# Optimization experiments

Measured on AMD Instinct MI355X. Metric: run time of the kernel, lower is better.

The kernel has to match this reference:

```python
import jax, jax.numpy as jnp
import numpy as np

NUM_VARS = 64
EDGE_TYPES = 4
HID = 128
IN = 32
BATCH = 64
SKIP_FIRST = True


def setup_inputs() -> dict:
    key = jax.random.key(0)
    ks = jax.random.split(key, 16)
    adj = np.ones((NUM_VARS, NUM_VARS)) - np.eye(NUM_VARS)
    send, recv = np.where(adj)  # [N*(N-1)] each
    E = send.shape[0]
    s = 0.05
    return {
        'inputs': jax.random.normal(ks[0], (BATCH, NUM_VARS, IN), jnp.float32),
        'edges': jax.random.uniform(ks[1], (BATCH, E, EDGE_TYPES), dtype=jnp.float32),
        'msg_fc1_w': jax.random.normal(ks[2], (EDGE_TYPES, HID, 2 * IN), jnp.float32) * s,
        'msg_fc1_b': jax.random.normal(ks[3], (EDGE_TYPES, HID), jnp.float32) * s,
        'msg_fc2_w': jax.random.normal(ks[4], (EDGE_TYPES, HID, HID), jnp.float32) * s,
        'msg_fc2_b': jax.random.normal(ks[5], (EDGE_TYPES, HID), jnp.float32) * s,
        'out_fc1_w': jax.random.normal(ks[6], (HID, IN + HID), jnp.float32) * s,
        'out_fc1_b': jax.random.normal(ks[7], (HID,), jnp.float32) * s,
        'out_fc2_w': jax.random.normal(ks[8], (HID, HID), jnp.float32) * s,
        'out_fc2_b': jax.random.normal(ks[9], (HID,), jnp.float32) * s,
        'mu_w': jax.random.normal(ks[10], (IN, HID), jnp.float32) * s,
        'mu_b': jax.random.normal(ks[11], (IN,), jnp.float32) * s,
        'logstd_w': jax.random.normal(ks[12], (IN, HID), jnp.float32) * s,
        'logstd_b': jax.random.normal(ks[13], (IN,), jnp.float32) * s,
        'send_edges': jnp.asarray(send, jnp.int32),
        'recv_edges': jnp.asarray(recv, jnp.int32),
    }


def reference(inputs, edges, msg_fc1_w, msg_fc1_b, msg_fc2_w, msg_fc2_b,
              out_fc1_w, out_fc1_b, out_fc2_w, out_fc2_b,
              mu_w, mu_b, logstd_w, logstd_b, send_edges, recv_edges):
    # gather receiver/sender node features per edge: [B, E, 2*D]
    receivers = inputs[:, recv_edges, :]
    senders = inputs[:, send_edges, :]
    pre_msg = jnp.concatenate([receivers, senders], axis=-1)
    B, E, _ = pre_msg.shape
    all_msgs = jnp.zeros((B, E, HID), pre_msg.dtype)
    start = 1 if SKIP_FIRST else 0
    for i in range(start, EDGE_TYPES):  # small fixed loop over structurally distinct MLPs
        m = jax.nn.relu(jnp.einsum('bej,hj->beh', pre_msg, msg_fc1_w[i]) + msg_fc1_b[i])
        m = jax.nn.relu(jnp.einsum('beh,oh->beo', m, msg_fc2_w[i]) + msg_fc2_b[i])
        all_msgs = all_msgs + m * edges[:, :, i:i + 1]
    # scatter-add messages to receiver nodes (replaces dense one-hot matmul)
    agg_msgs = jnp.zeros((B, NUM_VARS, HID), all_msgs.dtype).at[:, recv_edges, :].add(all_msgs)
    aug_inputs = jnp.concatenate([inputs, agg_msgs], axis=-1)
    pred = jax.nn.relu(aug_inputs @ out_fc1_w.T + out_fc1_b)
    pred = jax.nn.relu(pred @ out_fc2_w.T + out_fc2_b)
    mu = pred @ mu_w.T + mu_b
    log_std = jnp.clip(pred @ logstd_w.T + logstd_b, -3.0, 1.0)
    std = jnp.exp(log_std)  # eval mode: std_gating = 0, noise suppressed
    pred_out = mu  # mu + 0 * noise * std
    return inputs + pred_out
```

## Files before the change

### kernel.cpp

```cpp
#include <hip/hip_runtime.h>
#include <hip/hip_bf16.h>
#include <hip/hip_fp16.h>

#define B_ 64
#define V_ 64
#define E_ 4032
#define HID_ 128
#define IN_ 32
#define BV_ (B_ * V_)

typedef __attribute__((ext_vector_type(2))) _Float16 f16x2;
typedef __attribute__((ext_vector_type(8))) _Float16 f16x8;
typedef __attribute__((ext_vector_type(4))) float f32x4;

__device__ __forceinline__ f16x2 bc2(unsigned u) { return __builtin_bit_cast(f16x2, u); }
__device__ __forceinline__ unsigned bcu(f16x2 h) { return __builtin_bit_cast(unsigned, h); }

__global__ void __launch_bounds__(256) prep_all(
    const float* __restrict__ x, const float* __restrict__ w1,
    const float* __restrict__ b1, const float* __restrict__ w2,
    const float* __restrict__ edges, const float* __restrict__ fc1w,
    const float* __restrict__ fc2w, const float* __restrict__ muw,
    _Float16* __restrict__ h1r, _Float16* __restrict__ h1s,
    _Float16* __restrict__ w2f, float* __restrict__ ewT,
    float* __restrict__ fc1wT, float* __restrict__ fc2wT,
    float* __restrict__ muwT) {
  const int bid = blockIdx.x, t = threadIdx.x;

  if (bid < 2048) {
    __shared__ float xs[2][IN_];
    if (t < 64) xs[t >> 5][t & 31] = x[bid * 64 + t];
    __syncthreads();
    const int h = t & 127, half_ = t >> 7;
#pragma unroll
    for (int tt = 0; tt < 3; ++tt) {
      const float* wrow = w1 + ((size_t)((tt + 1) * HID_ + h)) * (2 * IN_) + half_ * IN_;
      float4 w[8];
#pragma unroll
      for (int j = 0; j < 8; ++j) w[j] = ((const float4*)wrow)[j];
      const float bias = half_ ? 0.f : b1[(tt + 1) * HID_ + h];
      _Float16* dst = (half_ ? h1s : h1r) + ((size_t)tt * BV_ + bid * 2) * HID_ + h;
#pragma unroll
      for (int n = 0; n < 2; ++n) {
        float acc = bias;
#pragma unroll
        for (int j = 0; j < 8; ++j)
          acc += w[j].x * xs[n][4 * j] + w[j].y * xs[n][4 * j + 1] +
                 w[j].z * xs[n][4 * j + 2] + w[j].w * xs[n][4 * j + 3];
        dst[n * HID_] = (_Float16)acc;
      }
    }
    return;
  }
  if (bid < 2240) {
    const int i = (bid - 2048) * 256 + t;
    const int e = i & 7, lane = (i >> 3) & 63, ks = (i >> 9) & 3;
    const int nt = (i >> 11) & 1, w = (i >> 12) & 3, tt = i >> 14;
    const int o = w * 32 + nt * 16 + (lane & 15);
    const int k = ks * 32 + (lane >> 4) * 8 + e;
    w2f[i] = (_Float16)w2[((size_t)((tt + 1) * HID_ + o)) * HID_ + k];
    return;
  }
  if (bid < 2400) {
    int j = (bid - 2240) * 256 + t;
    if (j < 20480) { fc1wT[j] = fc1w[(j & 127) * (IN_ + HID_) + (j >> 7)]; return; }
    j -= 20480;
    if (j < 16384) { fc2wT[j] = fc2w[(j & 127) * HID_ + (j >> 7)]; return; }
    j -= 16384;
    muwT[j] = muw[(j & 31) * HID_ + (j >> 5)];
    return;
  }
  {
    const int g = bid - 2400;
    if (t < 192) {
      const int b = g >> 6, v = g & 63;
      const int tt = t >> 6, r = t & 63;
      float val = 0.f;
      if (r < 63) {
        const int u = (r < v) ? r : r + 1;
        const int vv = (v > u) ? v - 1 : v;
        val = edges[((size_t)b * E_ + u * 63 + vv) * 4 + tt + 1];
      }
      ewT[(size_t)g * 192 + t] = val;
    }
    return;
  }
}

__global__ void __launch_bounds__(256)
edge_mfma(const float* __restrict__ b2, const _Float16* __restrict__ h1r,
          const _Float16* __restrict__ h1s, const _Float16* __restrict__ w2f,
          const float* __restrict__ ewT, float* __restrict__ aggout) {
  const int v = blockIdx.x, b = blockIdx.y, t = threadIdx.x;
  const int wave = t >> 6, lane = t & 63;
  const int l15 = lane & 15, lg = lane >> 4;
  const int kq = lane & 31, rpar = lane >> 5;

  __shared__ __align__(16) unsigned short m1[2][64 * HID_];
  __shared__ __align__(16) float ews[192];

  if (t < 192) ews[t] = ewT[((size_t)b * V_ + v) * 192 + t];

  {
    const unsigned short* hrp =
        (const unsigned short*)h1r + ((size_t)b * V_ + v) * HID_ + kq * 4;
    uint2 hru = *(const uint2*)hrp;
    const f16x2 hr0 = bc2(hru.x), hr1 = bc2(hru.y);
#pragma unroll
    for (int j = 0; j < 8; ++j) {
      const int r = wave * 16 + j * 2 + rpar;
      int u = (r < v) ? r : r + 1;
      if (r == 63) u = v;
      uint2 hsu = *(const uint2*)((const unsigned short*)h1s +
                                  ((size_t)b * V_ + u) * HID_ + kq * 4);
      f16x2 o0 = __builtin_elementwise_max(hr0 + bc2(hsu.x), (f16x2)0);
      f16x2 o1 = __builtin_elementwise_max(hr1 + bc2(hsu.y), (f16x2)0);
      uint2 pk = {bcu(o0), bcu(o1)};
      *(uint2*)((char*)m1[0] + r * 256 + ((kq * 8) ^ ((r & 7) << 4))) = pk;
    }
  }

  f16x8 bfrag[2][4];
  float b2r[2];
#pragma unroll
  for (int nt = 0; nt < 2; ++nt) {
#pragma unroll
    for (int ks = 0; ks < 4; ++ks)
      bfrag[nt][ks] = *(const f16x8*)(w2f + (((wave * 2 + nt) * 4 + ks) * 64 + lane) * 8);
    b2r[nt] = b2[HID_ + wave * 32 + nt * 16 + l15];
  }

  float acc[4][2][4];
#pragma unroll
  for (int mt = 0; mt < 4; ++mt)
#pragma unroll
    for (int nt = 0; nt < 2; ++nt)
#pragma unroll
      for (int r = 0; r < 4; ++r) acc[mt][nt][r] = 0.f;

  __syncthreads();

#pragma unroll
  for (int tt = 0; tt < 3; ++tt) {
    uint2 hrn, hsn[8];
    if (tt < 2) {
      hrn = *(const uint2*)((const unsigned short*)h1r +
                            ((size_t)((tt + 1) * B_ + b) * V_ + v) * HID_ + kq * 4);
#pragma unroll
      for (int j = 0; j < 8; ++j) {
        const int r = wave * 16 + j * 2 + rpar;
        int u = (r < v) ? r : r + 1;
        if (r == 63) u = v;
        hsn[j] = *(const uint2*)((const unsigned short*)h1s +
                                 ((size_t)((tt + 1) * B_ + b) * V_ + u) * HID_ + kq * 4);
      }
    }
    const unsigned short* mb = m1[tt & 1];
#pragma unroll
    for (int mt = 0; mt < 4; ++mt) {
      f16x8 af[4];
#pragma unroll
      for (int ks = 0; ks < 4; ++ks) {
        const int row = mt * 16 + l15;
        af[ks] = *(const f16x8*)((const char*)mb + row * 256 +
                                 ((ks * 64 + lg * 16) ^ ((row & 7) << 4)));
      }
      const float4 ew4 = *(const float4*)&ews[tt * 64 + mt * 16 + lg * 4];
#pragma unroll
      for (int nt = 0; nt < 2; ++nt) {
        f32x4 macc = {0.f, 0.f, 0.f, 0.f};
#pragma unroll
        for (int ks = 0; ks < 4; ++ks)
          macc = __builtin_amdgcn_mfma_f32_16x16x32_f16(af[ks], bfrag[nt][ks], macc, 0, 0, 0);
        acc[mt][nt][0] += fmaxf(macc[0] + b2r[nt], 0.f) * ew4.x;
        acc[mt][nt][1] += fmaxf(macc[1] + b2r[nt], 0.f) * ew4.y;
        acc[mt][nt][2] += fmaxf(macc[2] + b2r[nt], 0.f) * ew4.z;
        acc[mt][nt][3] += fmaxf(macc[3] + b2r[nt], 0.f) * ew4.w;
      }
    }
    if (tt < 2) {
      const f16x2 hr0 = bc2(hrn.x), hr1 = bc2(hrn.y);
#pragma unroll
      for (int j = 0; j < 8; ++j) {
        const int r = wave * 16 + j * 2 + rpar;
        f16x2 o0 = __builtin_elementwise_max(hr0 + bc2(hsn[j].x), (f16x2)0);
        f16x2 o1 = __builtin_elementwise_max(hr1 + bc2(hsn[j].y), (f16x2)0);
        uint2 pk = {bcu(o0), bcu(o1)};
        *(uint2*)((char*)m1[(tt + 1) & 1] + r * 256 + ((kq * 8) ^ ((r & 7) << 4))) = pk;
      }
#pragma unroll
      for (int nt = 0; nt < 2; ++nt) {
#pragma unroll
        for (int ks = 0; ks < 4; ++ks)
          bfrag[nt][ks] = *(const f16x8*)(
              w2f + (((((tt + 1) * 4 + wave) * 2 + nt) * 4 + ks) * 64 + lane) * 8);
        b2r[nt] = b2[(tt + 2) * HID_ + wave * 32 + nt * 16 + l15];
      }
    }
    __syncthreads();
  }

#pragma unroll
  for (int nt = 0; nt < 2; ++nt) {
    float s = 0.f;
#pragma unroll
    for (int mt = 0; mt < 4; ++mt)
#pragma unroll
      for (int r = 0; r < 4; ++r) s += acc[mt][nt][r];
    s += __shfl_xor(s, 16);
    s += __shfl_xor(s, 32);
    if (lane < 16)
      aggout[((size_t)b * V_ + v) * HID_ + wave * 32 + nt * 16 + l15] = s;
  }
}

__global__ void __launch_bounds__(256) out_mlp(
    const float* __restrict__ x, const float* __restrict__ aggout,
    const float* __restrict__ fc1wT, const float* __restrict__ fc1b,
    const float* __restrict__ fc2wT, const float* __restrict__ fc2b,
    const float* __restrict__ muwT, const float* __restrict__ mub,
    float* __restrict__ out) {
  const int t = threadIdx.x;
  const int g = t >> 5, j = t & 31;
  const int nodebase = blockIdx.x * 8;
  __shared__ __align__(16) float aug[8][164];
  __shared__ __align__(16) float p1[8][132];
  __shared__ __align__(16) float p2[8][132];

  aug[t >> 5][t & 31] = x[nodebase * IN_ + t];
  {
    float4 a4 = *(const float4*)(aggout + (size_t)nodebase * HID_ + t * 4);
    *(float4*)&aug[t >> 5][IN_ + (t & 31) * 4] = a4;
  }
  __syncthreads();

  float4 a1 = *(const float4*)(fc1b + j * 4);
#pragma unroll 4
  for (int k = 0; k < IN_ + HID_; ++k) {
    float4 w = *(const float4*)(fc1wT + (size_t)k * HID_ + j * 4);
    const float a = aug[g][k];
    a1.x += w.x * a; a1.y += w.y * a; a1.z += w.z * a; a1.w += w.w * a;
  }
  a1.x = fmaxf(a1.x, 0.f); a1.y = fmaxf(a1.y, 0.f);
  a1.z = fmaxf(a1.z, 0.f); a1.w = fmaxf(a1.w, 0.f);
  *(float4*)&p1[g][j * 4] = a1;
  __syncthreads();

  float4 a2 = *(const float4*)(fc2b + j * 4);
#pragma unroll 4
  for (int k = 0; k < HID_; ++k) {
    float4 w = *(const float4*)(fc2wT + (size_t)k * HID_ + j * 4);
    const float a = p1[g][k];
    a2.x += w.x * a; a2.y += w.y * a; a2.z += w.z * a; a2.w += w.w * a;
  }
  a2.x = fmaxf(a2.x, 0.f); a2.y = fmaxf(a2.y, 0.f);
  a2.z = fmaxf(a2.z, 0.f); a2.w = fmaxf(a2.w, 0.f);
  *(float4*)&p2[g][j * 4] = a2;
  __syncthreads();

  float am = mub[j];
#pragma unroll 4
  for (int k = 0; k < HID_; ++k) am += muwT[k * IN_ + j] * p2[g][k];
  out[(size_t)(nodebase + g) * IN_ + j] = aug[g][j] + am;
}

extern "C" void kernel_launch(void* const* d_in, const int* in_sizes, int n_in,
                              void* d_out, int out_size, void* d_ws, size_t ws_size,
                              hipStream_t stream) {
  const float* x     = (const float*)d_in[0];
  const float* edges = (const float*)d_in[1];
  const float* w1    = (const float*)d_in[2];
  const float* b1    = (const float*)d_in[3];
  const float* w2    = (const float*)d_in[4];
  const float* b2    = (const float*)d_in[5];
  const float* fc1w  = (const float*)d_in[6];
  const float* fc1b  = (const float*)d_in[7];
  const float* fc2w  = (const float*)d_in[8];
  const float* fc2b  = (const float*)d_in[9];
  const float* muw   = (const float*)d_in[10];
  const float* mub   = (const float*)d_in[11];
  float* out = (float*)d_out;

  float* aggout = (float*)d_ws;
  float* fc1wT  = aggout + BV_ * HID_;
  float* fc2wT  = fc1wT + (IN_ + HID_) * HID_;
  float* muwT   = fc2wT + HID_ * HID_;
  float* ewT    = muwT + HID_ * IN_;
  _Float16* h1r = (_Float16*)(ewT + (size_t)BV_ * 192);
  _Float16* h1s = h1r + (size_t)3 * BV_ * HID_;
  _Float16* w2f = h1s + (size_t)3 * BV_ * HID_;

  prep_all<<<6496, 256, 0, stream>>>(x, w1, b1, w2, edges, fc1w, fc2w, muw,
                                     h1r, h1s, w2f, ewT, fc1wT, fc2wT, muwT);
  edge_mfma<<<dim3(V_, B_), 256, 0, stream>>>(b2, h1r, h1s, w2f, ewT, aggout);
  out_mlp<<<512, 256, 0, stream>>>(x, aggout, fc1wT, fc1b, fc2wT, fc2b, muwT, mub, out);
}
```

Before: 183.3 us.

## Move output MLP to fp16 MFMA and drop LDS staging in edge kernel

```diff
diff --git a/kernel.cpp b/kernel.cpp
--- a/kernel.cpp
+++ b/kernel.cpp
@@ -9,12 +9,8 @@
 #define IN_ 32
 #define BV_ (B_ * V_)
 
-typedef __attribute__((ext_vector_type(2))) _Float16 f16x2;
 typedef __attribute__((ext_vector_type(8))) _Float16 f16x8;
 typedef __attribute__((ext_vector_type(4))) float f32x4;
-
-__device__ __forceinline__ f16x2 bc2(unsigned u) { return __builtin_bit_cast(f16x2, u); }
-__device__ __forceinline__ unsigned bcu(f16x2 h) { return __builtin_bit_cast(unsigned, h); }
 
 __global__ void __launch_bounds__(256) prep_all(
     const float* __restrict__ x, const float* __restrict__ w1,
@@ -22,9 +18,9 @@
     const float* __restrict__ edges, const float* __restrict__ fc1w,
     const float* __restrict__ fc2w, const float* __restrict__ muw,
     _Float16* __restrict__ h1r, _Float16* __restrict__ h1s,
-    _Float16* __restrict__ w2f, float* __restrict__ ewT,
-    float* __restrict__ fc1wT, float* __restrict__ fc2wT,
-    float* __restrict__ muwT) {
+    _Float16* __restrict__ w2f, _Float16* __restrict__ fc1f,
+    _Float16* __restrict__ fc2f, _Float16* __restrict__ muf,
+    _Float16* __restrict__ xh, float* __restrict__ ewT) {
   const int bid = blockIdx.x, t = threadIdx.x;
 
   if (bid < 2048) {
@@ -62,16 +58,43 @@
     return;
   }
   if (bid < 2400) {
-    int j = (bid - 2240) * 256 + t;
-    if (j < 20480) { fc1wT[j] = fc1w[(j & 127) * (IN_ + HID_) + (j >> 7)]; return; }
-    j -= 20480;
-    if (j < 16384) { fc2wT[j] = fc2w[(j & 127) * HID_ + (j >> 7)]; return; }
-    j -= 16384;
-    muwT[j] = muw[(j & 31) * HID_ + (j >> 5)];
+    int i = (bid - 2240) * 256 + t;
+    if (i < 20480) {
+      const int e = i & 7, lane = (i >> 3) & 63, rest = i >> 9;
+      const int ks = rest % 5, ntg = rest / 5;
+      const int o = ntg * 16 + (lane & 15);
+      const int k = ks * 32 + (lane >> 4) * 8 + e;
+      fc1f[i] = (_Float16)fc1w[(size_t)o * (IN_ + HID_) + k];
+      return;
+    }
+    i -= 20480;
+    if (i < 16384) {
+      const int e = i & 7, lane = (i >> 3) & 63, rest = i >> 9;
+      const int ks = rest & 3, ntg = rest >> 2;
+      const int o = ntg * 16 + (lane & 15);
+      const int k = ks * 32 + (lane >> 4) * 8 + e;
+      fc2f[i] = (_Float16)fc2w[(size_t)o * HID_ + k];
+      return;
+    }
+    i -= 16384;
+    {
+      const int e = i & 7, lane = (i >> 3) & 63, rest = i >> 9;
+      const int ks = rest & 3, ntg = rest >> 2;
+      const int o = ntg * 16 + (lane & 15);
+      const int k = ks * 32 + (lane >> 4) * 8 + e;
+      muf[i] = (_Float16)muw[(size_t)o * HID_ + k];
+      return;
+    }
+  }
+  if (bid < 2528) {
+    const int i4 = ((bid - 2400) * 256 + t) * 4;
+    float4 v4 = *(const float4*)(x + i4);
+    _Float16 o[4] = {(_Float16)v4.x, (_Float16)v4.y, (_Float16)v4.z, (_Float16)v4.w};
+    *(uint2*)(xh + i4) = *(const uint2*)o;
     return;
   }
   {
-    const int g = bid - 2400;
+    const int g = bid - 2528;
     if (t < 192) {
       const int b = g >> 6, v = g & 63;
       const int tt = t >> 6, r = t & 63;
@@ -87,117 +110,66 @@
   }
 }
 
-__global__ void __launch_bounds__(256)
+__global__ void __launch_bounds__(256, 4)
 edge_mfma(const float* __restrict__ b2, const _Float16* __restrict__ h1r,
           const _Float16* __restrict__ h1s, const _Float16* __restrict__ w2f,
-          const float* __restrict__ ewT, float* __restrict__ aggout) {
+          const float* __restrict__ ewT, _Float16* __restrict__ aggh) {
   const int v = blockIdx.x, b = blockIdx.y, t = threadIdx.x;
-  const int wave = t >> 6, lane = t & 63;
+  const int nh = t >> 6, lane = t & 63;
   const int l15 = lane & 15, lg = lane >> 4;
-  const int kq = lane & 31, rpar = lane >> 5;
-
-  __shared__ __align__(16) unsigned short m1[2][64 * HID_];
-  __shared__ __align__(16) float ews[192];
-
-  if (t < 192) ews[t] = ewT[((size_t)b * V_ + v) * 192 + t];
-
-  {
-    const unsigned short* hrp =
-        (const unsigned short*)h1r + ((size_t)b * V_ + v) * HID_ + kq * 4;
-    uint2 hru = *(const uint2*)hrp;
-    const f16x2 hr0 = bc2(hru.x), hr1 = bc2(hru.y);
-#pragma unroll
-    for (int j = 0; j < 8; ++j) {
-      const int r = wave * 16 + j * 2 + rpar;
+  const int bv = b * V_ + v;
+
+  float acc[4][2][4];
+#pragma unroll
+  for (int mt = 0; mt < 4; ++mt)
+#pragma unroll
+    for (int nt = 0; nt < 2; ++nt)
+#pragma unroll
+      for (int r = 0; r < 4; ++r) acc[mt][nt][r] = 0.f;
+
+#pragma unroll
+  for (int tt = 0; tt < 3; ++tt) {
+    const _Float16* hrp = h1r + ((size_t)(tt * B_ + b) * V_ + v) * HID_;
+    f16x8 hr[4];
+#pragma unroll
+    for (int ks = 0; ks < 4; ++ks) hr[ks] = *(const f16x8*)(hrp + ks * 32 + lg * 8);
+
+    f16x8 bf[2][4];
+    float b2r[2];
+#pragma unroll
+    for (int nt = 0; nt < 2; ++nt) {
+#pragma unroll
+      for (int ks = 0; ks < 4; ++ks)
+        bf[nt][ks] = *(const f16x8*)(
+            w2f + (size_t)(((((tt * 4 + nh) * 2 + nt) * 4 + ks) * 64 + lane)) * 8);
+      b2r[nt] = b2[(tt + 1) * HID_ + nh * 32 + nt * 16 + l15];
+    }
+
+    const _Float16* hsb = h1s + ((size_t)(tt * B_ + b) * V_) * HID_;
+#pragma unroll
+    for (int mt = 0; mt < 4; ++mt) {
+      const int r = mt * 16 + l15;
       int u = (r < v) ? r : r + 1;
       if (r == 63) u = v;
-      uint2 hsu = *(const uint2*)((const unsigned short*)h1s +
-                                  ((size_t)b * V_ + u) * HID_ + kq * 4);
-      f16x2 o0 = __builtin_elementwise_max(hr0 + bc2(hsu.x), (f16x2)0);
-      f16x2 o1 = __builtin_elementwise_max(hr1 + bc2(hsu.y), (f16x2)0);
-      uint2 pk = {bcu(o0), bcu(o1)};
-      *(uint2*)((char*)m1[0] + r * 256 + ((kq * 8) ^ ((r & 7) << 4))) = pk;
-    }
-  }
-
-  f16x8 bfrag[2][4];
-  float b2r[2];
-#pragma unroll
-  for (int nt = 0; nt < 2; ++nt) {
-#pragma unroll
-    for (int ks = 0; ks < 4; ++ks)
-      bfrag[nt][ks] = *(const f16x8*)(w2f + (((wave * 2 + nt) * 4 + ks) * 64 + lane) * 8);
-    b2r[nt] = b2[HID_ + wave * 32 + nt * 16 + l15];
-  }
-
-  float acc[4][2][4];
-#pragma unroll
-  for (int mt = 0; mt < 4; ++mt)
-#pragma unroll
-    for (int nt = 0; nt < 2; ++nt)
-#pragma unroll
-      for (int r = 0; r < 4; ++r) acc[mt][nt][r] = 0.f;
-
-  __syncthreads();
-
-#pragma unroll
-  for (int tt = 0; tt < 3; ++tt) {
-    uint2 hrn, hsn[8];
-    if (tt < 2) {
-      hrn = *(const uint2*)((const unsigned short*)h1r +
-                            ((size_t)((tt + 1) * B_ + b) * V_ + v) * HID_ + kq * 4);
-#pragma unroll
-      for (int j = 0; j < 8; ++j) {
-        const int r = wave * 16 + j * 2 + rpar;
-        int u = (r < v) ? r : r + 1;
-        if (r == 63) u = v;
-        hsn[j] = *(const uint2*)((const unsigned short*)h1s +
-                                 ((size_t)((tt + 1) * B_ + b) * V_ + u) * HID_ + kq * 4);
-      }
-    }
-    const unsigned short* mb = m1[tt & 1];
-#pragma unroll
-    for (int mt = 0; mt < 4; ++mt) {
       f16x8 af[4];
 #pragma unroll
       for (int ks = 0; ks < 4; ++ks) {
-        const int row = mt * 16 + l15;
-        af[ks] = *(const f16x8*)((const char*)mb + row * 256 +
-                                 ((ks * 64 + lg * 16) ^ ((row & 7) << 4)));
-      }
-      const float4 ew4 = *(const float4*)&ews[tt * 64 + mt * 16 + lg * 4];
+        f16x8 hs = *(const f16x8*)(hsb + (size_t)u * HID_ + ks * 32 + lg * 8);
+        af[ks] = __builtin_elementwise_max(hr[ks] + hs, (f16x8)0);
+      }
+      const float4 ew4 = *(const float4*)(ewT + (size_t)bv * 192 + tt * 64 + mt * 16 + lg * 4);
 #pragma unroll
       for (int nt = 0; nt < 2; ++nt) {
         f32x4 macc = {0.f, 0.f, 0.f, 0.f};
 #pragma unroll
         for (int ks = 0; ks < 4; ++ks)
-          macc = __builtin_amdgcn_mfma_f32_16x16x32_f16(af[ks], bfrag[nt][ks], macc, 0, 0, 0);
+          macc = __builtin_amdgcn_mfma_f32_16x16x32_f16(af[ks], bf[nt][ks], macc, 0, 0, 0);
         acc[mt][nt][0] += fmaxf(macc[0] + b2r[nt], 0.f) * ew4.x;
         acc[mt][nt][1] += fmaxf(macc[1] + b2r[nt], 0.f) * ew4.y;
         acc[mt][nt][2] += fmaxf(macc[2] + b2r[nt], 0.f) * ew4.z;
         acc[mt][nt][3] += fmaxf(macc[3] + b2r[nt], 0.f) * ew4.w;
       }
     }
-    if (tt < 2) {
-      const f16x2 hr0 = bc2(hrn.x), hr1 = bc2(hrn.y);
-#pragma unroll
-      for (int j = 0; j < 8; ++j) {
-        const int r = wave * 16 + j * 2 + rpar;
-        f16x2 o0 = __builtin_elementwise_max(hr0 + bc2(hsn[j].x), (f16x2)0);
-        f16x2 o1 = __builtin_elementwise_max(hr1 + bc2(hsn[j].y), (f16x2)0);
-        uint2 pk = {bcu(o0), bcu(o1)};
-        *(uint2*)((char*)m1[(tt + 1) & 1] + r * 256 + ((kq * 8) ^ ((r & 7) << 4))) = pk;
-      }
-#pragma unroll
-      for (int nt = 0; nt < 2; ++nt) {
-#pragma unroll
-        for (int ks = 0; ks < 4; ++ks)
-          bfrag[nt][ks] = *(const f16x8*)(
-              w2f + (((((tt + 1) * 4 + wave) * 2 + nt) * 4 + ks) * 64 + lane) * 8);
-        b2r[nt] = b2[(tt + 2) * HID_ + wave * 32 + nt * 16 + l15];
-      }
-    }
-    __syncthreads();
   }
 
 #pragma unroll
@@ -209,59 +181,86 @@
       for (int r = 0; r < 4; ++r) s += acc[mt][nt][r];
     s += __shfl_xor(s, 16);
     s += __shfl_xor(s, 32);
-    if (lane < 16)
-      aggout[((size_t)b * V_ + v) * HID_ + wave * 32 + nt * 16 + l15] = s;
-  }
-}
-
-__global__ void __launch_bounds__(256) out_mlp(
-    const float* __restrict__ x, const float* __restrict__ aggout,
-    const float* __restrict__ fc1wT, const float* __restrict__ fc1b,
-    const float* __restrict__ fc2wT, const float* __restrict__ fc2b,
-    const float* __restrict__ muwT, const float* __restrict__ mub,
-    float* __restrict__ out) {
+    if (lane < 16) aggh[(size_t)bv * HID_ + nh * 32 + nt * 16 + l15] = (_Float16)s;
+  }
+}
+
+__global__ void __launch_bounds__(256)
+out_mlp(const float* __restrict__ x, const _Float16* __restrict__ xh,
+        const _Float16* __restrict__ aggh, const _Float16* __restrict__ fc1f,
+        const float* __restrict__ fc1b, const _Float16* __restrict__ fc2f,
+        const float* __restrict__ fc2b, const _Float16* __restrict__ muf,
+        const float* __restrict__ mub, float* __restrict__ out) {
   const int t = threadIdx.x;
-  const int g = t >> 5, j = t & 31;
-  const int nodebase = blockIdx.x * 8;
-  __shared__ __align__(16) float aug[8][164];
-  __shared__ __align__(16) float p1[8][132];
-  __shared__ __align__(16) float p2[8][132];
-
-  aug[t >> 5][t & 31] = x[nodebase * IN_ + t];
-  {
-    float4 a4 = *(const float4*)(aggout + (size_t)nodebase * HID_ + t * 4);
-    *(float4*)&aug[t >> 5][IN_ + (t & 31) * 4] = a4;
+  const int lane = t & 63, l15 = lane & 15, lg = lane >> 4;
+  const int mh = (t >> 6) & 1, nh = t >> 7;
+  const int nb = blockIdx.x * 32;
+
+  __shared__ __align__(16) _Float16 p1h[32][136];
+  __shared__ __align__(16) _Float16 p2h[32][136];
+
+  const int arow = nb + mh * 16 + l15;
+  float4 acc1[4] = {{0, 0, 0, 0}, {0, 0, 0, 0}, {0, 0, 0, 0}, {0, 0, 0, 0}};
+#pragma unroll
+  for (int ks = 0; ks < 5; ++ks) {
+    f16x8 af = (ks == 0)
+                   ? *(const f16x8*)(xh + (size_t)arow * IN_ + lg * 8)
+                   : *(const f16x8*)(aggh + (size_t)arow * HID_ + (ks - 1) * 32 + lg * 8);
+#pragma unroll
+    for (int nt = 0; nt < 4; ++nt) {
+      f16x8 bf = *(const f16x8*)(fc1f + (size_t)((((nh * 4 + nt) * 5 + ks) * 64 + lane)) * 8);
+      *(f32x4*)&acc1[nt] =
+          __builtin_amdgcn_mfma_f32_16x16x32_f16(af, bf, *(f32x4*)&acc1[nt], 0, 0, 0);
+    }
+  }
+#pragma unroll
+  for (int nt = 0; nt < 4; ++nt) {
+    const int col = nh * 64 + nt * 16 + l15;
+    const float bias = fc1b[col];
+    p1h[mh * 16 + lg * 4 + 0][col] = (_Float16)fmaxf(acc1[nt].x + bias, 0.f);
+    p1h[mh * 16 + lg * 4 + 1][col] = (_Float16)fmaxf(acc1[nt].y + bias, 0.f);
+    p1h[mh * 16 + lg * 4 + 2][col] = (_Float16)fmaxf(acc1[nt].z + bias, 0.f);
+    p1h[mh * 16 + lg * 4 + 3][col] = (_Float16)fmaxf(acc1[nt].w + bias, 0.f);
   }
   __syncthreads();
 
-  float4 a1 = *(const float4*)(fc1b + j * 4);
-#pragma unroll 4
-  for (int k = 0; k < IN_ + HID_; ++k) {
-    float4 w = *(const float4*)(fc1wT + (size_t)k * HID_ + j * 4);
-    const float a = aug[g][k];
-    a1.x += w.x * a; a1.y += w.y * a; a1.z += w.z * a; a1.w += w.w * a;
-  }
-  a1.x = fmaxf(a1.x, 0.f); a1.y = fmaxf(a1.y, 0.f);
-  a1.z = fmaxf(a1.z, 0.f); a1.w = fmaxf(a1.w, 0.f);
-  *(float4*)&p1[g][j * 4] = a1;
+  float4 acc2[4] = {{0, 0, 0, 0}, {0, 0, 0, 0}, {0, 0, 0, 0}, {0, 0, 0, 0}};
+#pragma unroll
+  for (int ks = 0; ks < 4; ++ks) {
+    f16x8 af = *(const f16x8*)&p1h[mh * 16 + l15][ks * 32 + lg * 8];
+#pragma unroll
+    for (int nt = 0; nt < 4; ++nt) {
+      f16x8 bf = *(const f16x8*)(fc2f + (size_t)((((nh * 4 + nt) * 4 + ks) * 64 + lane)) * 8);
+      *(f32x4*)&acc2[nt] =
+          __builtin_amdgcn_mfma_f32_16x16x32_f16(af, bf, *(f32x4*)&acc2[nt], 0, 0, 0);
+    }
+  }
+#pragma unroll
+  for (int nt = 0; nt < 4; ++nt) {
+    const int col = nh * 64 + nt * 16 + l15;
+    const float bias = fc2b[col];
+    p2h[mh * 16 + lg * 4 + 0][col] = (_Float16)fmaxf(acc2[nt].x + bias, 0.f);
+    p2h[mh * 16 + lg * 4 + 1][col] = (_Float16)fmaxf(acc2[nt].y + bias, 0.f);
+    p2h[mh * 16 + lg * 4 + 2][col] = (_Float16)fmaxf(acc2[nt].z + bias, 0.f);
+    p2h[mh * 16 + lg * 4 + 3][col] = (_Float16)fmaxf(acc2[nt].w + bias, 0.f);
+  }
   __syncthreads();
 
-  float4 a2 = *(const float4*)(fc2b + j * 4);
-#pragma unroll 4
-  for (int k = 0; k < HID_; ++k) {
-    float4 w = *(const float4*)(fc2wT + (size_t)k * HID_ + j * 4);
-    const float a = p1[g][k];
-    a2.x += w.x * a; a2.y += w.y * a; a2.z += w.z * a; a2.w += w.w * a;
-  }
-  a2.x = fmaxf(a2.x, 0.f); a2.y = fmaxf(a2.y, 0.f);
-  a2.z = fmaxf(a2.z, 0.f); a2.w = fmaxf(a2.w, 0.f);
-  *(float4*)&p2[g][j * 4] = a2;
-  __syncthreads();
-
-  float am = mub[j];
-#pragma unroll 4
-  for (int k = 0; k < HID_; ++k) am += muwT[k * IN_ + j] * p2[g][k];
-  out[(size_t)(nodebase + g) * IN_ + j] = aug[g][j] + am;
+  float4 acc3 = {0, 0, 0, 0};
+#pragma unroll
+  for (int ks = 0; ks < 4; ++ks) {
+    f16x8 af = *(const f16x8*)&p2h[mh * 16 + l15][ks * 32 + lg * 8];
+    f16x8 bf = *(const f16x8*)(muf + (size_t)(((nh * 4 + ks) * 64 + lane)) * 8);
+    *(f32x4*)&acc3 = __builtin_amdgcn_mfma_f32_16x16x32_f16(af, bf, *(f32x4*)&acc3, 0, 0, 0);
+  }
+  const int col = nh * 16 + l15;
+  const float mb = mub[col];
+#pragma unroll
+  for (int r = 0; r < 4; ++r) {
+    const int node = nb + mh * 16 + lg * 4 + r;
+    out[(size_t)node * IN_ + col] =
+        x[(size_t)node * IN_ + col] + ((const float*)&acc3)[r] + mb;
+  }
 }
 
 extern "C" void kernel_launch(void* const* d_in, const int* in_sizes, int n_in,
@@ -281,17 +280,19 @@
   const float* mub   = (const float*)d_in[11];
   float* out = (float*)d_out;
 
-  float* aggout = (float*)d_ws;
-  float* fc1wT  = aggout + BV_ * HID_;
-  float* fc2wT  = fc1wT + (IN_ + HID_) * HID_;
-  float* muwT   = fc2wT + HID_ * HID_;
-  float* ewT    = muwT + HID_ * IN_;
+  float* ewT    = (float*)d_ws;
   _Float16* h1r = (_Float16*)(ewT + (size_t)BV_ * 192);
   _Float16* h1s = h1r + (size_t)3 * BV_ * HID_;
   _Float16* w2f = h1s + (size_t)3 * BV_ * HID_;
-
-  prep_all<<<6496, 256, 0, stream>>>(x, w1, b1, w2, edges, fc1w, fc2w, muw,
-                                     h1r, h1s, w2f, ewT, fc1wT, fc2wT, muwT);
-  edge_mfma<<<dim3(V_, B_), 256, 0, stream>>>(b2, h1r, h1s, w2f, ewT, aggout);
-  out_mlp<<<512, 256, 0, stream>>>(x, aggout, fc1wT, fc1b, fc2wT, fc2b, muwT, mub, out);
-}
+  _Float16* fc1f = w2f + 49152;
+  _Float16* fc2f = fc1f + 20480;
+  _Float16* muf  = fc2f + 16384;
+  _Float16* xh   = muf + 4096;
+  _Float16* aggh = xh + (size_t)BV_ * IN_;
+
+  prep_all<<<6624, 256, 0, stream>>>(x, w1, b1, w2, edges, fc1w, fc2w, muw,
+                                     h1r, h1s, w2f, fc1f, fc2f, muf, xh, ewT);
+  edge_mfma<<<dim3(V_, B_), 256, 0, stream>>>(b2, h1r, h1s, w2f, ewT, aggh);
+  out_mlp<<<BV_ / 32, 256, 0, stream>>>(x, xh, aggh, fc1f, fc1b, fc2f, fc2b,
+                                        muf, mub, out);
+}
```

Result: slower. 241.8 us (+31.9%).
